# Kernel tuning notes

Measured on AMD Instinct MI355X. Metric: run time of the kernel, lower is better.

## Reference

```python
import jax, jax.numpy as jnp
import numpy as np

B, S, D, H = 2, 2048, 1024, 16
HD = D // H

def setup_inputs() -> dict:
    key = jax.random.key(0)
    ks = jax.random.split(key, 5)
    sc = 1.0 / np.sqrt(D)
    return {
        "x": jax.random.normal(ks[0], (B, S, D), dtype=jnp.float32),
        "Wq": jax.random.normal(ks[1], (D, D), dtype=jnp.float32) * sc,
        "bq": jnp.zeros((D,), jnp.float32),
        "Wk": jax.random.normal(ks[2], (D, D), dtype=jnp.float32) * sc,
        "bk": jnp.zeros((D,), jnp.float32),
        "Wv": jax.random.normal(ks[3], (D, D), dtype=jnp.float32) * sc,
        "bv": jnp.zeros((D,), jnp.float32),
        "Wo": jax.random.normal(ks[4], (D, D), dtype=jnp.float32) * sc,
        "bo": jnp.zeros((D,), jnp.float32),
    }

def reference(x, Wq, bq, Wk, bk, Wv, bv, Wo, bo):
    b, s, d = x.shape
    def proj(W, bias):
        # [B,S,D] -> [B,H,S,HD]
        return (x @ W + bias).reshape(b, s, H, HD).swapaxes(1, 2)
    q = proj(Wq, bq)
    k = proj(Wk, bk)
    v = proj(Wv, bv)
    # naive full attention, matching the module (materializes [B,H,S,S])
    logits = jnp.einsum("bhqd,bhkd->bhqk", q, k) / jnp.sqrt(jnp.float32(HD))
    attn = jax.nn.softmax(logits, axis=-1)
    vals = jnp.einsum("bhqk,bhkd->bhqd", attn, v)
    vals = vals.swapaxes(1, 2).reshape(b, s, d)
    return vals @ Wo + bo
```

## Files before the change

kernel.cpp:

```cpp
#include <hip/hip_runtime.h>

typedef unsigned short u16;
typedef __bf16 bf16x8 __attribute__((ext_vector_type(8)));
typedef __bf16 bf16x4 __attribute__((ext_vector_type(4)));
typedef float f32x4 __attribute__((ext_vector_type(4)));

__device__ __forceinline__ u16 f2bf(float f) {
    union { float f; unsigned int i; } v;
    v.f = f;
    unsigned int u = v.i;
    return (u16)((u + 0x7fffu + ((u >> 16) & 1u)) >> 16);
}

__device__ __forceinline__ void dma16(const void* g, void* l) {
    __builtin_amdgcn_global_load_lds(
        (__attribute__((address_space(1))) void*)g,
        (__attribute__((address_space(3))) void*)l, 16, 0, 0);
}


__global__ __launch_bounds__(256) void cvt_w4(
    const float* __restrict__ W0, const float* __restrict__ W1,
    const float* __restrict__ W2, const float* __restrict__ W3,
    u16* __restrict__ out) {
    __shared__ u16 t[32][33];
    int z = blockIdx.z;
    const float* in = (z == 0) ? W0 : (z == 1) ? W1 : (z == 2) ? W2 : W3;
    u16* o = out + (size_t)z * 1048576;
    int bx = blockIdx.x * 32, by = blockIdx.y * 32;
    int tx = threadIdx.x & 31, ty = threadIdx.x >> 5;
#pragma unroll
    for (int i = 0; i < 32; i += 8)
        t[ty + i][tx] = f2bf(in[(size_t)(by + ty + i) * 1024 + bx + tx]);
    __syncthreads();
#pragma unroll
    for (int i = 0; i < 32; i += 8) {
        int n = bx + ty + i, k = by + tx;
        o[(size_t)n * 1024 + (k ^ ((n & 7) << 3))] = t[tx][ty + i];
    }
}

__global__ __launch_bounds__(256) void cvt_x(const float* __restrict__ in,
                                             u16* __restrict__ out) {
    int i = blockIdx.x * 256 + threadIdx.x;
    int s = i >> 8, k = (i & 255) * 4;
    float4 f = reinterpret_cast<const float4*>(in)[i];
    ushort4 h;
    h.x = f2bf(f.x); h.y = f2bf(f.y); h.z = f2bf(f.z); h.w = f2bf(f.w);
    *reinterpret_cast<ushort4*>(&out[(size_t)s * 1024 + (k ^ ((s & 7) << 3))]) = h;
}

__global__ __launch_bounds__(256) void gemm_qkv(
    const u16* __restrict__ xbf, const u16* __restrict__ wt,
    const float* __restrict__ bq, const float* __restrict__ bk,
    const float* __restrict__ bv,
    u16* __restrict__ qkg, u16* __restrict__ vgt) {
    __shared__ __align__(16) u16 As[128 * 64];
    __shared__ __align__(16) u16 Bs[128 * 64];

    int tid = threadIdx.x;
    int m0 = blockIdx.y * 128, n0 = blockIdx.x * 128;
    int wave = tid >> 6, lane = tid & 63;
    int wm = (wave >> 1) * 64, wn = (wave & 1) * 64;
    int l16 = lane & 15, quad = lane >> 4;
    int sl = l16 & 7;

    int seg = n0 >> 10;
    int n0r = n0 & 1023;
    const u16* WT = wt + (size_t)seg * 1048576;
    bool swp = (seg == 2);

    f32x4 acc[4][4];
#pragma unroll
    for (int mi = 0; mi < 4; mi++)
#pragma unroll
        for (int ni = 0; ni < 4; ni++) acc[mi][ni] = (f32x4){0.f, 0.f, 0.f, 0.f};

    int rsub = lane >> 3, c16 = (lane & 7) * 8;
    for (int k0 = 0; k0 < 1024; k0 += 64) {
#pragma unroll
        for (int i = 0; i < 4; i++) {
            int row = wave * 32 + i * 8 + rsub;
            dma16(&xbf[(size_t)(m0 + row) * 1024 + k0 + c16], &As[wave * 2048 + i * 512]);
            dma16(&WT[(size_t)(n0r + row) * 1024 + k0 + c16], &Bs[wave * 2048 + i * 512]);
        }
        __syncthreads();
        const u16* Am = swp ? Bs : As;
        const u16* Bn = swp ? As : Bs;
#pragma unroll
        for (int kk = 0; kk < 64; kk += 32) {
            int co = ((((kk >> 3) + quad) ^ sl) << 3);
            bf16x8 af[4], bf[4];
#pragma unroll
            for (int mi = 0; mi < 4; mi++)
                af[mi] = *reinterpret_cast<const bf16x8*>(
                    &Am[(wm + mi * 16 + l16) * 64 + co]);
#pragma unroll
            for (int ni = 0; ni < 4; ni++)
                bf[ni] = *reinterpret_cast<const bf16x8*>(
                    &Bn[(wn + ni * 16 + l16) * 64 + co]);
#pragma unroll
            for (int mi = 0; mi < 4; mi++)
#pragma unroll
                for (int ni = 0; ni < 4; ni++)
                    acc[mi][ni] = __builtin_amdgcn_mfma_f32_16x16x32_bf16(
                        af[mi], bf[ni], acc[mi][ni], 0, 0, 0);
        }
        __syncthreads();
    }

    if (!swp) {
#pragma unroll
        for (int ni = 0; ni < 4; ni++) {
            int n = n0 + wn + ni * 16 + l16;
            float bb = (n < 1024) ? bq[n] : bk[n - 1024];
#pragma unroll
            for (int mi = 0; mi < 4; mi++)
#pragma unroll
                for (int r = 0; r < 4; r++) {
                    int s = m0 + wm + mi * 16 + quad * 4 + r;
                    int key = (seg == 0) ? (s & 7) : ((s >> 2) & 7);
                    int col = n ^ (key << 3);
                    qkg[(size_t)(s >> 11) * 4194304 + (size_t)(s & 2047) * 2048 + col] =
                        f2bf(acc[mi][ni][r] + bb);
                }
        }
    } else {
#pragma unroll
        for (int mi = 0; mi < 4; mi++)
#pragma unroll
            for (int r = 0; r < 4; r++) {
                int v = n0r + wm + mi * 16 + quad * 4 + r;
                float bb = bv[v];
#pragma unroll
                for (int ni = 0; ni < 4; ni++) {
                    int s = m0 + wn + ni * 16 + l16;
                    int scol = (s & 2047) ^ ((v & 7) << 3);
                    vgt[(size_t)((s >> 11) * 1024 + v) * 2048 + scol] =
                        f2bf(acc[mi][ni][r] + bb);
                }
            }
    }
}

#define SC2 0.18033688f

__global__ __launch_bounds__(256) void attention_kern(
    u16* __restrict__ qkg, const u16* __restrict__ vgt) {
    __shared__ __align__(16) u16 Qs[64 * 64];
    __shared__ __align__(16) u16 Ks[64 * 64];
    __shared__ __align__(16) u16 Vt[64 * 64];
    __shared__ __align__(16) u16 Ps[64 * 64];

    int tid = threadIdx.x;
    int qt = blockIdx.x, h = blockIdx.y, b = blockIdx.z;
    int wave = tid >> 6, lane = tid & 63;
    int l16 = lane & 15, quad = lane >> 4;
    int rsub = lane >> 3, c16 = (lane & 7) * 8;
    int sl = l16 & 7;

    u16* qb = qkg + (size_t)b * 4194304 + (size_t)(qt * 64) * 2048 + h * 64;
    const u16* kb = qkg + (size_t)b * 4194304 + 1024 + h * 64;
    const u16* vb = vgt + (size_t)(b * 1024 + h * 64) * 2048;

#pragma unroll
    for (int i = 0; i < 2; i++) {
        int row = wave * 16 + i * 8 + rsub;
        dma16(&qb[(size_t)row * 2048 + c16], &Qs[wave * 1024 + i * 512]);
    }

    float lp[4];
    f32x4 o[4];
#pragma unroll
    for (int r = 0; r < 4; r++) lp[r] = 0.f;
#pragma unroll
    for (int ni = 0; ni < 4; ni++) o[ni] = (f32x4){0.f, 0.f, 0.f, 0.f};

    for (int kt = 0; kt < 32; kt++) {
        const u16* ktb = kb + (size_t)(kt * 64) * 2048;
        const u16* vtb = vb + kt * 64;
#pragma unroll
        for (int i = 0; i < 2; i++) {
            int gk = 32 * i + 4 * rsub + wave;
            dma16(&ktb[(size_t)gk * 2048 + c16], &Ks[wave * 1024 + i * 512]);
            int rv = wave * 16 + i * 8 + rsub;
            dma16(&vtb[(size_t)rv * 2048 + c16], &Vt[wave * 1024 + i * 512]);
        }
        __syncthreads();

        f32x4 s[4];
#pragma unroll
        for (int ni = 0; ni < 4; ni++) s[ni] = (f32x4){0.f, 0.f, 0.f, 0.f};
#pragma unroll
        for (int kk = 0; kk < 64; kk += 32) {
            int co = ((((kk >> 3) + quad) ^ sl) << 3);
            bf16x8 af = *reinterpret_cast<const bf16x8*>(
                &Qs[(wave * 16 + l16) * 64 + co]);
#pragma unroll
            for (int ni = 0; ni < 4; ni++) {
                bf16x8 bf = *reinterpret_cast<const bf16x8*>(
                    &Ks[(ni * 16 + l16) * 64 + co]);
                s[ni] = __builtin_amdgcn_mfma_f32_16x16x32_bf16(af, bf, s[ni], 0, 0, 0);
            }
        }

#pragma unroll
        for (int r = 0; r < 4; r++) {
            float p0 = __builtin_amdgcn_exp2f(s[0][r] * SC2);
            float p1 = __builtin_amdgcn_exp2f(s[1][r] * SC2);
            float p2 = __builtin_amdgcn_exp2f(s[2][r] * SC2);
            float p3 = __builtin_amdgcn_exp2f(s[3][r] * SC2);
            lp[r] += (p0 + p1) + (p2 + p3);
            f32x4 pf = {p0, p1, p2, p3};
            bf16x4 pb = __builtin_convertvector(pf, bf16x4);
            int q = wave * 16 + quad * 4 + r;
            *reinterpret_cast<bf16x4*>(
                &Ps[q * 64 + (((l16 >> 1) ^ (q & 7)) << 3) + (l16 & 1) * 4]) = pb;
        }

#pragma unroll
        for (int kk = 0; kk < 64; kk += 32) {
            int co = ((((kk >> 3) + quad) ^ sl) << 3);
            bf16x8 af = *reinterpret_cast<const bf16x8*>(
                &Ps[(wave * 16 + l16) * 64 + co]);
#pragma unroll
            for (int ni = 0; ni < 4; ni++) {
                bf16x8 bf = *reinterpret_cast<const bf16x8*>(
                    &Vt[(ni * 16 + l16) * 64 + co]);
                o[ni] = __builtin_amdgcn_mfma_f32_16x16x32_bf16(af, bf, o[ni], 0, 0, 0);
            }
        }
        __syncthreads();
    }

    float inv[4];
#pragma unroll
    for (int r = 0; r < 4; r++) {
        float v = lp[r];
#pragma unroll
        for (int off = 1; off < 16; off <<= 1) v += __shfl_xor(v, off);
        inv[r] = __builtin_amdgcn_rcpf(v);
    }
#pragma unroll
    for (int ni = 0; ni < 4; ni++)
#pragma unroll
        for (int r = 0; r < 4; r++) {
            int s = qt * 64 + wave * 16 + quad * 4 + r;
            int d = h * 64 + ni * 16 + l16;
            qkg[(size_t)b * 4194304 + (size_t)s * 2048 + (d ^ ((s & 7) << 3))] =
                f2bf(o[ni][r] * inv[r]);
        }
}

__global__ __launch_bounds__(256) void gemm_out(
    const u16* __restrict__ attb, const u16* __restrict__ wot,
    const float* __restrict__ bo, float* __restrict__ out) {
    __shared__ __align__(16) u16 As[128 * 64];
    __shared__ __align__(16) u16 Bs[64 * 64];

    int tid = threadIdx.x;
    int m0 = blockIdx.y * 128, n0 = blockIdx.x * 64;
    int wave = tid >> 6, lane = tid & 63;
    int wm = (wave >> 1) * 64, wn = (wave & 1) * 32;
    int l16 = lane & 15, quad = lane >> 4;
    int sl = l16 & 7;
    int rsub = lane >> 3, c16 = (lane & 7) * 8;

    f32x4 acc[4][2];
#pragma unroll
    for (int mi = 0; mi < 4; mi++)
#pragma unroll
        for (int ni = 0; ni < 2; ni++) acc[mi][ni] = (f32x4){0.f, 0.f, 0.f, 0.f};

    for (int k0 = 0; k0 < 1024; k0 += 64) {
#pragma unroll
        for (int i = 0; i < 4; i++) {
            int row = wave * 32 + i * 8 + rsub;
            dma16(&attb[(size_t)(m0 + row) * 2048 + k0 + c16], &As[wave * 2048 + i * 512]);
        }
#pragma unroll
        for (int i = 0; i < 2; i++) {
            int row = wave * 16 + i * 8 + rsub;
            dma16(&wot[(size_t)(n0 + row) * 1024 + k0 + c16], &Bs[wave * 1024 + i * 512]);
        }
        __syncthreads();
#pragma unroll
        for (int kk = 0; kk < 64; kk += 32) {
            int co = ((((kk >> 3) + quad) ^ sl) << 3);
            bf16x8 af[4], bf[2];
#pragma unroll
            for (int mi = 0; mi < 4; mi++)
                af[mi] = *reinterpret_cast<const bf16x8*>(
                    &As[(wm + mi * 16 + l16) * 64 + co]);
#pragma unroll
            for (int ni = 0; ni < 2; ni++)
                bf[ni] = *reinterpret_cast<const bf16x8*>(
                    &Bs[(wn + ni * 16 + l16) * 64 + co]);
#pragma unroll
            for (int mi = 0; mi < 4; mi++)
#pragma unroll
                for (int ni = 0; ni < 2; ni++)
                    acc[mi][ni] = __builtin_amdgcn_mfma_f32_16x16x32_bf16(
                        af[mi], bf[ni], acc[mi][ni], 0, 0, 0);
        }
        __syncthreads();
    }

#pragma unroll
    for (int ni = 0; ni < 2; ni++) {
        int n = n0 + wn + ni * 16 + l16;
        float bb = bo[n];
#pragma unroll
        for (int mi = 0; mi < 4; mi++)
#pragma unroll
            for (int r = 0; r < 4; r++)
                out[(size_t)(m0 + wm + mi * 16 + quad * 4 + r) * 1024 + n] =
                    acc[mi][ni][r] + bb;
    }
}

extern "C" void kernel_launch(void* const* d_in, const int* in_sizes, int n_in,
                              void* d_out, int out_size, void* d_ws, size_t ws_size,
                              hipStream_t stream) {
    const float* x  = (const float*)d_in[0];
    const float* Wq = (const float*)d_in[1];
    const float* bq = (const float*)d_in[2];
    const float* Wk = (const float*)d_in[3];
    const float* bk = (const float*)d_in[4];
    const float* Wv = (const float*)d_in[5];
    const float* bv = (const float*)d_in[6];
    const float* Wo = (const float*)d_in[7];
    const float* bo = (const float*)d_in[8];

    u16* WT  = (u16*)d_out;
    u16* xbf = (u16*)d_out + 4 * 1048576;
    u16* QKg = (u16*)d_ws;
    u16* Vgt = (u16*)d_ws + 8 * 1048576;

    cvt_w4<<<dim3(32, 32, 4), 256, 0, stream>>>(Wq, Wk, Wv, Wo, WT);
    cvt_x<<<4096, 256, 0, stream>>>(x, xbf);

    gemm_qkv<<<dim3(24, 32), 256, 0, stream>>>(xbf, WT, bq, bk, bv, QKg, Vgt);

    attention_kern<<<dim3(32, 16, 2), 256, 0, stream>>>(QKg, Vgt);

    hipMemcpyAsync(Vgt, WT + 3 * 1048576, (size_t)2 * 1048576,
                   hipMemcpyDeviceToDevice, stream);
    gemm_out<<<dim3(16, 32), 256, 0, stream>>>(QKg, Vgt, bo, (float*)d_out);
}
```

Baseline: 209.3 us.

## Double-buffer K/V and GEMM tiles; fold softmax scale into Q projection

The attention kernel and the output GEMM now use two shared-memory buffers for their K/V (resp. A/B) tiles. The next tile's async global-to-LDS copy is issued right after the barrier, so it overlaps the current tile's MFMA work, and one barrier per iteration is removed. The exp2 softmax scale is folded into the Q projection epilogue, which removes a multiply per score in the inner loop. In exchange, LDS use per block grows, and Q is now scaled before bf16 rounding, which slightly changes numerics.

```diff
diff --git a/kernel.cpp b/kernel.cpp
--- a/kernel.cpp
+++ b/kernel.cpp
@@ -17,6 +17,8 @@
         (__attribute__((address_space(1))) void*)g,
         (__attribute__((address_space(3))) void*)l, 16, 0, 0);
 }
+
+#define SC2 0.18033688f
 
 
 __global__ __launch_bounds__(256) void cvt_w4(
@@ -110,6 +112,7 @@
     }
 
     if (!swp) {
+        float scale = (seg == 0) ? SC2 : 1.0f;
 #pragma unroll
         for (int ni = 0; ni < 4; ni++) {
             int n = n0 + wn + ni * 16 + l16;
@@ -122,7 +125,7 @@
                     int key = (seg == 0) ? (s & 7) : ((s >> 2) & 7);
                     int col = n ^ (key << 3);
                     qkg[(size_t)(s >> 11) * 4194304 + (size_t)(s & 2047) * 2048 + col] =
-                        f2bf(acc[mi][ni][r] + bb);
+                        f2bf((acc[mi][ni][r] + bb) * scale);
                 }
         }
     } else {
@@ -143,13 +146,11 @@
     }
 }
 
-#define SC2 0.18033688f
-
 __global__ __launch_bounds__(256) void attention_kern(
     u16* __restrict__ qkg, const u16* __restrict__ vgt) {
     __shared__ __align__(16) u16 Qs[64 * 64];
-    __shared__ __align__(16) u16 Ks[64 * 64];
-    __shared__ __align__(16) u16 Vt[64 * 64];
+    __shared__ __align__(16) u16 Ks[2][64 * 64];
+    __shared__ __align__(16) u16 Vt[2][64 * 64];
     __shared__ __align__(16) u16 Ps[64 * 64];
 
     int tid = threadIdx.x;
@@ -169,6 +170,18 @@
         dma16(&qb[(size_t)row * 2048 + c16], &Qs[wave * 1024 + i * 512]);
     }
 
+    {
+        const u16* ktb = kb;
+        const u16* vtb = vb;
+#pragma unroll
+        for (int i = 0; i < 2; i++) {
+            int gk = 32 * i + 4 * rsub + wave;
+            dma16(&ktb[(size_t)gk * 2048 + c16], &Ks[0][wave * 1024 + i * 512]);
+            int rv = wave * 16 + i * 8 + rsub;
+            dma16(&vtb[(size_t)rv * 2048 + c16], &Vt[0][wave * 1024 + i * 512]);
+        }
+    }
+
     float lp[4];
     f32x4 o[4];
 #pragma unroll
@@ -177,16 +190,21 @@
     for (int ni = 0; ni < 4; ni++) o[ni] = (f32x4){0.f, 0.f, 0.f, 0.f};
 
     for (int kt = 0; kt < 32; kt++) {
-        const u16* ktb = kb + (size_t)(kt * 64) * 2048;
-        const u16* vtb = vb + kt * 64;
-#pragma unroll
-        for (int i = 0; i < 2; i++) {
-            int gk = 32 * i + 4 * rsub + wave;
-            dma16(&ktb[(size_t)gk * 2048 + c16], &Ks[wave * 1024 + i * 512]);
-            int rv = wave * 16 + i * 8 + rsub;
-            dma16(&vtb[(size_t)rv * 2048 + c16], &Vt[wave * 1024 + i * 512]);
-        }
         __syncthreads();
+
+        if (kt < 31) {
+            int nb = (kt + 1) & 1;
+            const u16* ktb = kb + (size_t)((kt + 1) * 64) * 2048;
+            const u16* vtb = vb + (kt + 1) * 64;
+#pragma unroll
+            for (int i = 0; i < 2; i++) {
+                int gk = 32 * i + 4 * rsub + wave;
+                dma16(&ktb[(size_t)gk * 2048 + c16], &Ks[nb][wave * 1024 + i * 512]);
+                int rv = wave * 16 + i * 8 + rsub;
+                dma16(&vtb[(size_t)rv * 2048 + c16], &Vt[nb][wave * 1024 + i * 512]);
+            }
+        }
+        int cb = kt & 1;
 
         f32x4 s[4];
 #pragma unroll
@@ -199,17 +217,17 @@
 #pragma unroll
             for (int ni = 0; ni < 4; ni++) {
                 bf16x8 bf = *reinterpret_cast<const bf16x8*>(
-                    &Ks[(ni * 16 + l16) * 64 + co]);
+                    &Ks[cb][(ni * 16 + l16) * 64 + co]);
                 s[ni] = __builtin_amdgcn_mfma_f32_16x16x32_bf16(af, bf, s[ni], 0, 0, 0);
             }
         }
 
 #pragma unroll
         for (int r = 0; r < 4; r++) {
-            float p0 = __builtin_amdgcn_exp2f(s[0][r] * SC2);
-            float p1 = __builtin_amdgcn_exp2f(s[1][r] * SC2);
-            float p2 = __builtin_amdgcn_exp2f(s[2][r] * SC2);
-            float p3 = __builtin_amdgcn_exp2f(s[3][r] * SC2);
+            float p0 = __builtin_amdgcn_exp2f(s[0][r]);
+            float p1 = __builtin_amdgcn_exp2f(s[1][r]);
+            float p2 = __builtin_amdgcn_exp2f(s[2][r]);
+            float p3 = __builtin_amdgcn_exp2f(s[3][r]);
             lp[r] += (p0 + p1) + (p2 + p3);
             f32x4 pf = {p0, p1, p2, p3};
             bf16x4 pb = __builtin_convertvector(pf, bf16x4);
@@ -226,11 +244,10 @@
 #pragma unroll
             for (int ni = 0; ni < 4; ni++) {
                 bf16x8 bf = *reinterpret_cast<const bf16x8*>(
-                    &Vt[(ni * 16 + l16) * 64 + co]);
+                    &Vt[cb][(ni * 16 + l16) * 64 + co]);
                 o[ni] = __builtin_amdgcn_mfma_f32_16x16x32_bf16(af, bf, o[ni], 0, 0, 0);
             }
         }
-        __syncthreads();
     }
 
     float inv[4];
@@ -255,8 +272,8 @@
 __global__ __launch_bounds__(256) void gemm_out(
     const u16* __restrict__ attb, const u16* __restrict__ wot,
     const float* __restrict__ bo, float* __restrict__ out) {
-    __shared__ __align__(16) u16 As[128 * 64];
-    __shared__ __align__(16) u16 Bs[64 * 64];
+    __shared__ __align__(16) u16 As[2][128 * 64];
+    __shared__ __align__(16) u16 Bs[2][64 * 64];
 
     int tid = threadIdx.x;
     int m0 = blockIdx.y * 128, n0 = blockIdx.x * 64;
@@ -272,18 +289,35 @@
 #pragma unroll
         for (int ni = 0; ni < 2; ni++) acc[mi][ni] = (f32x4){0.f, 0.f, 0.f, 0.f};
 
-    for (int k0 = 0; k0 < 1024; k0 += 64) {
-#pragma unroll
-        for (int i = 0; i < 4; i++) {
-            int row = wave * 32 + i * 8 + rsub;
-            dma16(&attb[(size_t)(m0 + row) * 2048 + k0 + c16], &As[wave * 2048 + i * 512]);
-        }
-#pragma unroll
-        for (int i = 0; i < 2; i++) {
-            int row = wave * 16 + i * 8 + rsub;
-            dma16(&wot[(size_t)(n0 + row) * 1024 + k0 + c16], &Bs[wave * 1024 + i * 512]);
-        }
+#pragma unroll
+    for (int i = 0; i < 4; i++) {
+        int row = wave * 32 + i * 8 + rsub;
+        dma16(&attb[(size_t)(m0 + row) * 2048 + c16], &As[0][wave * 2048 + i * 512]);
+    }
+#pragma unroll
+    for (int i = 0; i < 2; i++) {
+        int row = wave * 16 + i * 8 + rsub;
+        dma16(&wot[(size_t)(n0 + row) * 1024 + c16], &Bs[0][wave * 1024 + i * 512]);
+    }
+
+    for (int it = 0; it < 16; it++) {
         __syncthreads();
+        if (it < 15) {
+            int nb = (it + 1) & 1, k0 = (it + 1) * 64;
+#pragma unroll
+            for (int i = 0; i < 4; i++) {
+                int row = wave * 32 + i * 8 + rsub;
+                dma16(&attb[(size_t)(m0 + row) * 2048 + k0 + c16],
+                      &As[nb][wave * 2048 + i * 512]);
+            }
+#pragma unroll
+            for (int i = 0; i < 2; i++) {
+                int row = wave * 16 + i * 8 + rsub;
+                dma16(&wot[(size_t)(n0 + row) * 1024 + k0 + c16],
+                      &Bs[nb][wave * 1024 + i * 512]);
+            }
+        }
+        int cb = it & 1;
 #pragma unroll
         for (int kk = 0; kk < 64; kk += 32) {
             int co = ((((kk >> 3) + quad) ^ sl) << 3);
@@ -291,11 +325,11 @@
 #pragma unroll
             for (int mi = 0; mi < 4; mi++)
                 af[mi] = *reinterpret_cast<const bf16x8*>(
-                    &As[(wm + mi * 16 + l16) * 64 + co]);
+                    &As[cb][(wm + mi * 16 + l16) * 64 + co]);
 #pragma unroll
             for (int ni = 0; ni < 2; ni++)
                 bf[ni] = *reinterpret_cast<const bf16x8*>(
-                    &Bs[(wn + ni * 16 + l16) * 64 + co]);
+                    &Bs[cb][(wn + ni * 16 + l16) * 64 + co]);
 #pragma unroll
             for (int mi = 0; mi < 4; mi++)
 #pragma unroll
@@ -303,7 +337,6 @@
                     acc[mi][ni] = __builtin_amdgcn_mfma_f32_16x16x32_bf16(
                         af[mi], bf[ni], acc[mi][ni], 0, 0, 0);
         }
-        __syncthreads();
     }
 
 #pragma unroll
```

Result: slower. 241.6 us (+15.4%).
